# Kernel tuning notes

Measured on AMD Instinct MI355X. Metric: run time of the kernel, lower is better.

Reference implementation:

```python
import jax, jax.numpy as jnp
import numpy as np

B, DIM, EMBDIM = 32, 512, 512
MEMSIZE, MEMSEQ = 32, 64
VOCAB = 50257


def setup_inputs() -> dict:
    key = jax.random.key(0)
    ks = jax.random.split(key, 10)
    inp = {
        'enc': jax.random.normal(ks[0], (B, DIM), jnp.float32),
        'encsumm': jax.random.normal(ks[1], (B, DIM), jnp.float32),
        'embsumm': jax.random.normal(ks[2], (B, EMBDIM), jnp.float32),
        'memencs': jax.random.normal(ks[3], (B, MEMSIZE, MEMSEQ, DIM), jnp.float32),
        'memencsumm': jax.random.normal(ks[4], (B, MEMSIZE, MEMSEQ, DIM), jnp.float32),
        'memembsumm': jax.random.normal(ks[5], (B, MEMSIZE, MEMSEQ, EMBDIM), jnp.float32),
        'memmask': jnp.ones((B, MEMSIZE, MEMSEQ), jnp.float32),
        'memids': jax.random.randint(ks[6], (B, MEMSIZE, MEMSEQ), 0, VOCAB, jnp.int64 if jax.config.jax_enable_x64 else jnp.int32),
        'W_out': jax.random.normal(ks[7], (VOCAB, 2 * DIM), jnp.float32) * 0.02,
        'b_out': jnp.zeros((VOCAB,), jnp.float32),
        'W_mix': jax.random.normal(ks[8], (2, 2 * DIM), jnp.float32) * 0.02,
        'b_mix': jnp.zeros((2,), jnp.float32),
        'unktok_mask': jnp.ones((VOCAB,), jnp.float32),  # no unktoks
    }
    return inp


def reference(enc, encsumm, embsumm, memencs, memencsumm, memembsumm, memmask,
              memids, W_out, b_out, W_mix, b_mix, unktok_mask):
    # copy branch: attention over flattened memory, scatter-add into vocab
    query = jnp.concatenate([embsumm, jnp.zeros_like(encsumm), enc], axis=-1)        # (B, 2*dim+embdim)
    keys = jnp.concatenate([memembsumm, jnp.zeros_like(memencsumm), memencs], axis=-1)  # (B, M, Z, 2*dim+embdim)
    w = jnp.einsum('bd,bmzd->bmz', query, keys) + jnp.log(memmask)
    b = w.shape[0]
    w = w.reshape(b, -1)                                    # (B, M*Z)
    alphas = jax.nn.softmax(w, axis=-1)
    mem_flat = memencs.reshape(b, -1, memencs.shape[-1])    # (B, M*Z, dim)
    mem_enc_summ = jnp.einsum('bm,bmd->bd', alphas, mem_flat)
    toks = memids.reshape(b, -1)                            # (B, M*Z)
    rows = jnp.arange(b)[:, None]
    vocsize = W_out.shape[0]
    probs_mem = jnp.zeros((b, vocsize), alphas.dtype).at[rows, toks].add(alphas)
    # generation branch
    h = jnp.concatenate([encsumm, enc], axis=-1)            # (B, 2*dim)
    logits_gen = h @ W_out.T + b_out + jnp.log(unktok_mask)[None, :]
    probs_gen = jax.nn.softmax(logits_gen, axis=-1)
    # mixer combine
    mix = jax.nn.softmax(h @ W_mix.T + b_mix, axis=-1)      # (B, 2)
    probs = mix[:, 0:1] * probs_gen + mix[:, 1:2] * probs_mem
    # original stack/gather trick: selects probs where nonzero, zeros where zero -> identity
    probs = jnp.where(probs != 0, probs, jnp.zeros_like(probs))
    return probs, mem_enc_summ
```

## Files before the change

### kernel.cpp

```cpp
#include <hip/hip_runtime.h>
#include <hip/hip_bf16.h>

#define NB   32
#define DIMK 512
#define MM   32
#define ZZ   64
#define MZV  2048
#define VOC  50257

typedef __attribute__((ext_vector_type(8))) short  short8;
typedef __attribute__((ext_vector_type(4))) float  f32x4;
typedef __attribute__((ext_vector_type(8))) unsigned short ushort8;

#define WS_W      0
#define WS_PVEC   (WS_W + NB*MZV)
#define WS_LSTAT  (WS_PVEC + NB*MM*DIMK)
#define WS_GSTATW (WS_LSTAT + NB*MM*2)
#define WS_MIX    (WS_GSTATW + NB*2)
#define WS_GPART  (WS_MIX + NB*2)
#define WS_H      (WS_GPART + NB*32*2)

__device__ __forceinline__ ushort8 cvt8(float4 a, float4 b) {
    union { ushort8 u; __hip_bfloat162 h[4]; } r;
    r.h[0] = __float22bfloat162_rn(make_float2(a.x, a.y));
    r.h[1] = __float22bfloat162_rn(make_float2(a.z, a.w));
    r.h[2] = __float22bfloat162_rn(make_float2(b.x, b.y));
    r.h[3] = __float22bfloat162_rn(make_float2(b.z, b.w));
    return r.u;
}

__global__ void k0_stageh(const float* __restrict__ encsumm, const float* __restrict__ enc,
                          float* __restrict__ ws)
{
    int b = blockIdx.x;
    int c = threadIdx.x * 4;
    const float* src = (c < DIMK) ? (encsumm + b*DIMK + c) : (enc + b*DIMK + (c - DIMK));
    float4 v = *(const float4*)src;
    union { ushort4 u; __hip_bfloat162 h[2]; } o;
    o.h[0] = __float22bfloat162_rn(make_float2(v.x, v.y));
    o.h[1] = __float22bfloat162_rn(make_float2(v.z, v.w));
    *(ushort4*)((unsigned short*)(ws + WS_H) + b*1024 + c) = o.u;
}

__global__ __launch_bounds__(256) void k1_mem(
    const float* __restrict__ enc, const float* __restrict__ embsumm,
    const float* __restrict__ memencs, const float* __restrict__ memembsumm,
    const float* __restrict__ memmask, float* __restrict__ ws)
{
    int blk = blockIdx.x;
    int b = blk >> 5, m = blk & 31;
    int tid = threadIdx.x, wid = tid >> 6, lane = tid & 63;
    int c0 = lane * 4, c1 = c0 + 256;
    const float* encb = enc + b * DIMK;
    const float* embb = embsumm + b * DIMK;
    float4 qe0 = *(const float4*)(encb + c0);
    float4 qe1 = *(const float4*)(encb + c1);
    float4 qm0 = *(const float4*)(embb + c0);
    float4 qm1 = *(const float4*)(embb + c1);
    const float* meb = memencs    + (long)(b*MM + m) * ZZ * DIMK;
    const float* mmb = memembsumm + (long)(b*MM + m) * ZZ * DIMK;
    const float* mkb = memmask    + (long)(b*MM + m) * ZZ;
    float* w_ws = ws + WS_W + b*MZV + m*ZZ;

    float lmax = -3.0e38f, lsum = 0.f;
    float4 a0 = make_float4(0.f,0.f,0.f,0.f), a1 = make_float4(0.f,0.f,0.f,0.f);

    for (int z = wid; z < ZZ; z += 4) {
        const float* mer = meb + z*DIMK;
        const float* mmr = mmb + z*DIMK;
        float4 e0 = *(const float4*)(mer + c0);
        float4 e1 = *(const float4*)(mer + c1);
        float4 s0 = *(const float4*)(mmr + c0);
        float4 s1 = *(const float4*)(mmr + c1);
        float d = e0.x*qe0.x + e0.y*qe0.y + e0.z*qe0.z + e0.w*qe0.w
                + e1.x*qe1.x + e1.y*qe1.y + e1.z*qe1.z + e1.w*qe1.w
                + s0.x*qm0.x + s0.y*qm0.y + s0.z*qm0.z + s0.w*qm0.w
                + s1.x*qm1.x + s1.y*qm1.y + s1.z*qm1.z + s1.w*qm1.w;
        #pragma unroll
        for (int off = 32; off; off >>= 1) d += __shfl_xor(d, off);
        d += logf(mkb[z]);
        if (lane == 0) w_ws[z] = d;
        float nm = fmaxf(lmax, d);
        float sc = __expf(lmax - nm);
        float e  = __expf(d - nm);
        lsum = lsum * sc + e;
        a0.x = a0.x*sc + e*e0.x; a0.y = a0.y*sc + e*e0.y;
        a0.z = a0.z*sc + e*e0.z; a0.w = a0.w*sc + e*e0.w;
        a1.x = a1.x*sc + e*e1.x; a1.y = a1.y*sc + e*e1.y;
        a1.z = a1.z*sc + e*e1.z; a1.w = a1.w*sc + e*e1.w;
        lmax = nm;
    }

    __shared__ float sacc[4][DIMK];
    __shared__ float sst[4][2];
    *(float4*)&sacc[wid][c0] = a0;
    *(float4*)&sacc[wid][c1] = a1;
    if (lane == 0) { sst[wid][0] = lmax; sst[wid][1] = lsum; }
    __syncthreads();
    float bm = fmaxf(fmaxf(sst[0][0], sst[1][0]), fmaxf(sst[2][0], sst[3][0]));
    float sc0 = __expf(sst[0][0]-bm), sc1 = __expf(sst[1][0]-bm);
    float sc2 = __expf(sst[2][0]-bm), sc3 = __expf(sst[3][0]-bm);
    float bs = sst[0][1]*sc0 + sst[1][1]*sc1 + sst[2][1]*sc2 + sst[3][1]*sc3;
    int d0 = tid * 2;
    float2 v0 = *(float2*)&sacc[0][d0];
    float2 v1 = *(float2*)&sacc[1][d0];
    float2 v2 = *(float2*)&sacc[2][d0];
    float2 v3 = *(float2*)&sacc[3][d0];
    float p0 = v0.x*sc0 + v1.x*sc1 + v2.x*sc2 + v3.x*sc3;
    float p1 = v0.y*sc0 + v1.y*sc1 + v2.y*sc2 + v3.y*sc3;
    float* pv = ws + WS_PVEC + (long)(b*MM+m)*DIMK + d0;
    pv[0] = p0; pv[1] = p1;
    if (tid == 0) { float* ls = ws + WS_LSTAT + (b*MM+m)*2; ls[0] = bm; ls[1] = bs; }
}

__global__ __launch_bounds__(256) void k2_comb(float* __restrict__ out, float* __restrict__ ws)
{
    int b = blockIdx.x, tid = threadIdx.x;
    const float* ls = ws + WS_LSTAT + b*MM*2;
    float gm = -3.0e38f;
    #pragma unroll
    for (int m = 0; m < MM; m++) gm = fmaxf(gm, ls[m*2]);
    float gs = 0.f;
    #pragma unroll
    for (int m = 0; m < MM; m++) gs += ls[m*2+1] * __expf(ls[m*2] - gm);
    if (tid == 0) { ws[WS_GSTATW + b*2] = gm; ws[WS_GSTATW + b*2 + 1] = gs; }
    float inv = 1.0f / gs;
    int d0 = tid * 2;
    float p0 = 0.f, p1 = 0.f;
    for (int m = 0; m < MM; m++) {
        float sc = __expf(ls[m*2] - gm);
        const float* pv = ws + WS_PVEC + (long)(b*MM+m)*DIMK + d0;
        p0 += pv[0]*sc; p1 += pv[1]*sc;
    }
    out[(long)NB*VOC + b*DIMK + d0]     = p0 * inv;
    out[(long)NB*VOC + b*DIMK + d0 + 1] = p1 * inv;
}

__global__ void k3_mix(const float* __restrict__ encsumm, const float* __restrict__ enc,
                       const float* __restrict__ W_mix, const float* __restrict__ b_mix,
                       float* __restrict__ ws)
{
    int b = blockIdx.x, l = threadIdx.x;
    float d0 = 0.f, d1 = 0.f;
    #pragma unroll
    for (int p = 0; p < 4; p++) {
        int cc = l*4 + p*256;
        float4 h4 = (cc < 512) ? *(const float4*)(encsumm + b*DIMK + cc)
                               : *(const float4*)(enc + b*DIMK + cc - 512);
        float4 w0 = *(const float4*)(W_mix + cc);
        float4 w1 = *(const float4*)(W_mix + 1024 + cc);
        d0 += h4.x*w0.x + h4.y*w0.y + h4.z*w0.z + h4.w*w0.w;
        d1 += h4.x*w1.x + h4.y*w1.y + h4.z*w1.z + h4.w*w1.w;
    }
    #pragma unroll
    for (int off = 32; off; off >>= 1) { d0 += __shfl_xor(d0, off); d1 += __shfl_xor(d1, off); }
    if (l == 0) {
        d0 += b_mix[0]; d1 += b_mix[1];
        float mx = fmaxf(d0, d1);
        float e0 = __expf(d0-mx), e1 = __expf(d1-mx);
        float s = e0 + e1;
        ws[WS_MIX + b*2] = e0/s; ws[WS_MIX + b*2 + 1] = e1/s;
    }
}

__global__ __launch_bounds__(256) void k4_gemm(
    const unsigned short* __restrict__ hbf,
    const float* __restrict__ W_out, const float* __restrict__ b_out,
    const float* __restrict__ unk, float* __restrict__ logits)
{
    __shared__ __align__(16) unsigned short b_lds[16*64*8];
    __shared__ __align__(16) unsigned short a_lds[16*32*8];
    int tid = threadIdx.x, wid = tid >> 6, lane = tid & 63;
    int vt = blockIdx.x * 64;

    int r = tid >> 2;
    int q = tid & 3;
    long grow = min(vt + r, VOC - 1);
    const float* wbase = W_out + grow * 1024 + q * 32;

    int ar0 = tid >> 4, ag0 = tid & 15;
    int ar1 = (tid + 256) >> 4, ag1 = ag0;

    int lg = lane >> 4;
    int ln = lane & 15;

    f32x4 acc0 = {0.f,0.f,0.f,0.f};
    f32x4 acc1 = {0.f,0.f,0.f,0.f};

    for (int c = 0; c < 8; ++c) {
        int kc = c * 128;
        ushort8 av0 = *(const ushort8*)(hbf + ar0*1024 + kc + ag0*8);
        ushort8 av1 = *(const ushort8*)(hbf + ar1*1024 + kc + ag1*8);
        *(ushort8*)&a_lds[(ag0*32 + (ar0 ^ (ag0 & 7)))*8] = av0;
        *(ushort8*)&a_lds[(ag1*32 + (ar1 ^ (ag1 & 7)))*8] = av1;
        const float* wp = wbase + kc;
        float4 f0 = *(const float4*)(wp +  0);
        float4 f1 = *(const float4*)(wp +  4);
        float4 f2 = *(const float4*)(wp +  8);
        float4 f3 = *(const float4*)(wp + 12);
        float4 f4 = *(const float4*)(wp + 16);
        float4 f5 = *(const float4*)(wp + 20);
        float4 f6 = *(const float4*)(wp + 24);
        float4 f7 = *(const float4*)(wp + 28);
        *(ushort8*)&b_lds[((q*4 + 0)*64 + r)*8] = cvt8(f0, f1);
        *(ushort8*)&b_lds[((q*4 + 1)*64 + r)*8] = cvt8(f2, f3);
        *(ushort8*)&b_lds[((q*4 + 2)*64 + r)*8] = cvt8(f4, f5);
        *(ushort8*)&b_lds[((q*4 + 3)*64 + r)*8] = cvt8(f6, f7);
        __syncthreads();
        #pragma unroll
        for (int s = 0; s < 4; ++s) {
            int g = s*4 + lg;
            short8 bfrag = *(const short8*)&b_lds[(g*64 + wid*16 + ln)*8];
            short8 a0 = *(const short8*)&a_lds[(g*32 + (ln ^ (g & 7)))*8];
            short8 a1 = *(const short8*)&a_lds[(g*32 + ((ln + 16) ^ (g & 7)))*8];
            acc0 = __builtin_amdgcn_mfma_f32_16x16x32_bf16(a0, bfrag, acc0, 0, 0, 0);
            acc1 = __builtin_amdgcn_mfma_f32_16x16x32_bf16(a1, bfrag, acc1, 0, 0, 0);
        }
        __syncthreads();
    }

    int v = vt + wid*16 + ln;
    if (v < VOC) {
        float bias = b_out[v] + logf(unk[v]);
        #pragma unroll
        for (int rr = 0; rr < 4; ++rr) {
            int m = lg*4 + rr;
            logits[(long)m*VOC + v]        = acc0[rr] + bias;
            logits[(long)(m+16)*VOC + v]   = acc1[rr] + bias;
        }
    }
}

__global__ __launch_bounds__(256) void k5_gstat(const float* __restrict__ logits, float* __restrict__ ws)
{
    int chunk = blockIdx.x, b = blockIdx.y, tid = threadIdx.x;
    const int CH = (VOC + 31) / 32;
    int v0 = chunk * CH;
    int v1 = min(VOC, v0 + CH);
    float m = -3.0e38f, s = 0.f;
    for (int v = v0 + tid; v < v1; v += 256) {
        float x = logits[(long)b*VOC + v];
        float nm = fmaxf(m, x);
        s = s*__expf(m - nm) + __expf(x - nm);
        m = nm;
    }
    #pragma unroll
    for (int off = 32; off; off >>= 1) {
        float om = __shfl_xor(m, off), os = __shfl_xor(s, off);
        float nm = fmaxf(m, om);
        s = s*__expf(m - nm) + os*__expf(om - nm);
        m = nm;
    }
    __shared__ float sm[4], ssum[4];
    int wid = tid >> 6, lane = tid & 63;
    if (lane == 0) { sm[wid] = m; ssum[wid] = s; }
    __syncthreads();
    if (tid == 0) {
        float gm = fmaxf(fmaxf(sm[0], sm[1]), fmaxf(sm[2], sm[3]));
        float gs = ssum[0]*__expf(sm[0]-gm) + ssum[1]*__expf(sm[1]-gm)
                 + ssum[2]*__expf(sm[2]-gm) + ssum[3]*__expf(sm[3]-gm);
        ws[WS_GPART + (b*32 + chunk)*2]     = gm;
        ws[WS_GPART + (b*32 + chunk)*2 + 1] = gs;
    }
}

__global__ __launch_bounds__(256) void k6_final(float* __restrict__ probs, const float* __restrict__ ws)
{
    int v = blockIdx.x*256 + threadIdx.x;
    int b = blockIdx.y;
    float gm = -3.0e38f;
    #pragma unroll
    for (int i = 0; i < 32; ++i) gm = fmaxf(gm, ws[WS_GPART + (b*32+i)*2]);
    float gs = 0.f;
    #pragma unroll
    for (int i = 0; i < 32; ++i)
        gs += ws[WS_GPART + (b*32+i)*2 + 1] * __expf(ws[WS_GPART + (b*32+i)*2] - gm);
    if (v >= VOC) return;
    float mix0 = ws[WS_MIX + b*2];
    long idx = (long)b*VOC + v;
    probs[idx] = mix0 * __expf(probs[idx] - gm) / gs;
}

__global__ __launch_bounds__(256) void k7_scatter(const int* __restrict__ memids,
                                                  const float* __restrict__ ws,
                                                  float* __restrict__ probs)
{
    int idx = blockIdx.x*256 + threadIdx.x;
    int b = idx >> 11, mz = idx & 2047;
    float gm = ws[WS_GSTATW + b*2], gs = ws[WS_GSTATW + b*2 + 1];
    float mix1 = ws[WS_MIX + b*2 + 1];
    float alpha = __expf(ws[WS_W + b*MZV + mz] - gm) / gs;
    int tok = memids[b*MZV + mz];
    atomicAdd(&probs[(long)b*VOC + tok], mix1 * alpha);
}

extern "C" void kernel_launch(void* const* d_in, const int* in_sizes, int n_in,
                              void* d_out, int out_size, void* d_ws, size_t ws_size,
                              hipStream_t stream)
{
    const float* enc        = (const float*)d_in[0];
    const float* encsumm    = (const float*)d_in[1];
    const float* embsumm    = (const float*)d_in[2];
    const float* memencs    = (const float*)d_in[3];
    const float* memembsumm = (const float*)d_in[5];
    const float* memmask    = (const float*)d_in[6];
    const int*   memids     = (const int*)d_in[7];
    const float* W_out      = (const float*)d_in[8];
    const float* b_out      = (const float*)d_in[9];
    const float* W_mix      = (const float*)d_in[10];
    const float* b_mix      = (const float*)d_in[11];
    const float* unk        = (const float*)d_in[12];
    float* out = (float*)d_out;
    float* ws  = (float*)d_ws;

    hipLaunchKernelGGL(k0_stageh, dim3(NB), dim3(256), 0, stream, encsumm, enc, ws);
    hipLaunchKernelGGL(k1_mem, dim3(NB*MM), dim3(256), 0, stream,
                       enc, embsumm, memencs, memembsumm, memmask, ws);
    hipLaunchKernelGGL(k2_comb, dim3(NB), dim3(256), 0, stream, out, ws);
    hipLaunchKernelGGL(k3_mix, dim3(NB), dim3(64), 0, stream, encsumm, enc, W_mix, b_mix, ws);
    hipLaunchKernelGGL(k4_gemm, dim3((VOC + 63)/64), dim3(256), 0, stream,
                       (const unsigned short*)(ws + WS_H), W_out, b_out, unk, out);
    hipLaunchKernelGGL(k5_gstat, dim3(32, NB), dim3(256), 0, stream, out, ws);
    hipLaunchKernelGGL(k6_final, dim3((VOC + 255)/256, NB), dim3(256), 0, stream, out, ws);
    hipLaunchKernelGGL(k7_scatter, dim3(NB*MZV/256), dim3(256), 0, stream, memids, ws, out);
}
```

Measured before the change: 139.5 us.

## Double-buffer LDS and prefetch W_out chunks in vocab GEMM kernel

Restructures the k4_gemm K-loop into 16 chunks of 64 with double-buffered LDS tiles. The next chunk's global loads are issued while MFMAs run on the current buffer, leaving one barrier per iteration. It also adds an XOR swizzle on the B tile to cut LDS bank conflicts. The aim is to hide global load latency of the large fp32 W_out stream, at the cost of more registers and smaller per-iteration work.

```diff
diff --git a/kernel.cpp b/kernel.cpp
--- a/kernel.cpp
+++ b/kernel.cpp
@@ -168,58 +168,64 @@
     const float* __restrict__ W_out, const float* __restrict__ b_out,
     const float* __restrict__ unk, float* __restrict__ logits)
 {
-    __shared__ __align__(16) unsigned short b_lds[16*64*8];
-    __shared__ __align__(16) unsigned short a_lds[16*32*8];
+    __shared__ __align__(16) unsigned short b_lds[2][8*64*8];
+    __shared__ __align__(16) unsigned short a_lds[2][8*32*8];
     int tid = threadIdx.x, wid = tid >> 6, lane = tid & 63;
     int vt = blockIdx.x * 64;
 
-    int r = tid >> 2;
-    int q = tid & 3;
+    int r = tid >> 2, q = tid & 3;
     long grow = min(vt + r, VOC - 1);
-    const float* wbase = W_out + grow * 1024 + q * 32;
-
-    int ar0 = tid >> 4, ag0 = tid & 15;
-    int ar1 = (tid + 256) >> 4, ag1 = ag0;
-
-    int lg = lane >> 4;
-    int ln = lane & 15;
+    const float* wbase = W_out + grow * 1024 + q * 16;
+    int ar = tid >> 3, ag = tid & 7;
+    const unsigned short* abase = hbf + ar * 1024 + ag * 8;
+
+    int lg = lane >> 4, ln = lane & 15;
+    int vrow = wid*16 + ln;
 
     f32x4 acc0 = {0.f,0.f,0.f,0.f};
     f32x4 acc1 = {0.f,0.f,0.f,0.f};
-
-    for (int c = 0; c < 8; ++c) {
-        int kc = c * 128;
-        ushort8 av0 = *(const ushort8*)(hbf + ar0*1024 + kc + ag0*8);
-        ushort8 av1 = *(const ushort8*)(hbf + ar1*1024 + kc + ag1*8);
-        *(ushort8*)&a_lds[(ag0*32 + (ar0 ^ (ag0 & 7)))*8] = av0;
-        *(ushort8*)&a_lds[(ag1*32 + (ar1 ^ (ag1 & 7)))*8] = av1;
-        const float* wp = wbase + kc;
-        float4 f0 = *(const float4*)(wp +  0);
-        float4 f1 = *(const float4*)(wp +  4);
-        float4 f2 = *(const float4*)(wp +  8);
-        float4 f3 = *(const float4*)(wp + 12);
-        float4 f4 = *(const float4*)(wp + 16);
-        float4 f5 = *(const float4*)(wp + 20);
-        float4 f6 = *(const float4*)(wp + 24);
-        float4 f7 = *(const float4*)(wp + 28);
-        *(ushort8*)&b_lds[((q*4 + 0)*64 + r)*8] = cvt8(f0, f1);
-        *(ushort8*)&b_lds[((q*4 + 1)*64 + r)*8] = cvt8(f2, f3);
-        *(ushort8*)&b_lds[((q*4 + 2)*64 + r)*8] = cvt8(f4, f5);
-        *(ushort8*)&b_lds[((q*4 + 3)*64 + r)*8] = cvt8(f6, f7);
-        __syncthreads();
+    float4 f0, f1, f2, f3; ushort8 av;
+
+    int g0 = 2*q, g1 = 2*q + 1;
+    int bw0 = (g0*64 + (r ^ ((g0 & 3) << 2))) * 8;
+    int bw1 = (g1*64 + (r ^ ((g1 & 3) << 2))) * 8;
+    int aw  = (ag*32 + (ar ^ ag)) * 8;
+
+#define LOADC(c) do { const float* wp = wbase + (c)*64;              \
+        f0 = *(const float4*)(wp);      f1 = *(const float4*)(wp+4); \
+        f2 = *(const float4*)(wp+8);    f3 = *(const float4*)(wp+12);\
+        av = *(const ushort8*)(abase + (c)*64); } while (0)
+#define WRITEC(buf) do {                                \
+        *(ushort8*)&b_lds[buf][bw0] = cvt8(f0, f1);     \
+        *(ushort8*)&b_lds[buf][bw1] = cvt8(f2, f3);     \
+        *(ushort8*)&a_lds[buf][aw]  = av; } while (0)
+
+    LOADC(0); WRITEC(0);
+    LOADC(1);
+    __syncthreads();
+
+    #pragma unroll 2
+    for (int c = 0; c < 16; ++c) {
+        int buf = c & 1;
         #pragma unroll
-        for (int s = 0; s < 4; ++s) {
+        for (int s = 0; s < 2; ++s) {
             int g = s*4 + lg;
-            short8 bfrag = *(const short8*)&b_lds[(g*64 + wid*16 + ln)*8];
-            short8 a0 = *(const short8*)&a_lds[(g*32 + (ln ^ (g & 7)))*8];
-            short8 a1 = *(const short8*)&a_lds[(g*32 + ((ln + 16) ^ (g & 7)))*8];
+            short8 bfrag = *(const short8*)&b_lds[buf][(g*64 + (vrow ^ ((g & 3) << 2)))*8];
+            short8 a0 = *(const short8*)&a_lds[buf][(g*32 + (ln ^ g))*8];
+            short8 a1 = *(const short8*)&a_lds[buf][(g*32 + ((ln + 16) ^ g))*8];
             acc0 = __builtin_amdgcn_mfma_f32_16x16x32_bf16(a0, bfrag, acc0, 0, 0, 0);
             acc1 = __builtin_amdgcn_mfma_f32_16x16x32_bf16(a1, bfrag, acc1, 0, 0, 0);
         }
+        if (c < 15) {
+            WRITEC(buf ^ 1);
+            if (c < 14) LOADC(c + 2);
+        }
         __syncthreads();
     }
-
-    int v = vt + wid*16 + ln;
+#undef LOADC
+#undef WRITEC
+
+    int v = vt + vrow;
     if (v < VOC) {
         float bias = b_out[v] + logf(unk[v]);
         #pragma unroll
```

Result: no change. 138.1 us (-1.0%).
